# Performance work log

Hardware: AMD Instinct MI355X
Metric: run time of the kernel (lower is better)

Reference implementation:

```python
import jax, jax.numpy as jnp
from jax import lax
import numpy as np

B, T, F, H = 4096, 512, 8, 16  # batch, seq, n_features, hidden_dim


def _lstm(x, Wih, Whh, bih, bhh):
    """PyTorch-convention LSTM over batch-first x [B,T,in].
    Returns (h_T [B,H], outputs [B,T,H]). Gate order: i, f, g, o."""
    Bn = x.shape[0]
    Hn = Whh.shape[1]
    xs = jnp.swapaxes(x, 0, 1)                       # [T,B,in]
    x_proj = xs @ Wih.T + (bih + bhh)                # precompute input GEMM: [T,B,4H]

    def step(carry, xp):
        h, c = carry
        gates = xp + h @ Whh.T                       # [B,4H]
        i, f, g, o = jnp.split(gates, 4, axis=-1)
        i = jax.nn.sigmoid(i)
        f = jax.nn.sigmoid(f)
        g = jnp.tanh(g)
        o = jax.nn.sigmoid(o)
        c = f * c + i * g
        h = o * jnp.tanh(c)
        return (h, c), h

    h0 = jnp.zeros((Bn, Hn), x.dtype)
    (hT, _), hs = lax.scan(step, (h0, h0), x_proj)
    return hT, jnp.swapaxes(hs, 0, 1)                # [B,H], [B,T,H]


def setup_inputs() -> dict:
    key = jax.random.key(0)
    ks = jax.random.split(key, 11)
    s_e = 1.0 / np.sqrt(H)
    u = lambda k, shp: jax.random.uniform(k, shp, jnp.float32, -s_e, s_e)
    return {
        "x": jax.random.normal(ks[0], (B, T, F), jnp.float32),
        "enc_Wih": u(ks[1], (4 * H, F)),
        "enc_Whh": u(ks[2], (4 * H, H)),
        "enc_bih": u(ks[3], (4 * H,)),
        "enc_bhh": u(ks[4], (4 * H,)),
        "dec_Wih": u(ks[5], (4 * H, H)),
        "dec_Whh": u(ks[6], (4 * H, H)),
        "dec_bih": u(ks[7], (4 * H,)),
        "dec_bhh": u(ks[8], (4 * H,)),
        "out_W": u(ks[9], (F, H)),
        "out_b": u(ks[10], (F,)),
    }


def reference(x, enc_Wih, enc_Whh, enc_bih, enc_bhh,
              dec_Wih, dec_Whh, dec_bih, dec_bhh, out_W, out_b):
    # encoder: keep only final hidden state h_T
    hT, _ = _lstm(x, enc_Wih, enc_Whh, enc_bih, enc_bhh)   # [B,H]
    # repeat over time: h.squeeze(0).unsqueeze(1).repeat(1,T,1)
    repeated = jnp.broadcast_to(hT[:, None, :], (x.shape[0], x.shape[1], hT.shape[1]))
    _, decoded = _lstm(repeated, dec_Wih, dec_Whh, dec_bih, dec_bhh)  # [B,T,H]
    return decoded @ out_W.T + out_b                       # [B,T,F]
```

## Files before the change

### kernel.cpp

```cpp
#include <hip/hip_runtime.h>

#define B_ 4096
#define T_ 512
#define F_ 8
#define H_ 16

typedef float f32x2 __attribute__((ext_vector_type(2)));

__device__ __forceinline__ f32x2 pkfma(f32x2 a, f32x2 b, f32x2 c) {
    return __builtin_elementwise_fma(a, b, c);
}

__device__ __forceinline__ float sigf(float v) {
    return __builtin_amdgcn_rcpf(1.0f + __expf(-v));
}
__device__ __forceinline__ float tanh_f(float v) {
    return 2.0f * __builtin_amdgcn_rcpf(1.0f + __expf(-2.0f * v)) - 1.0f;
}

__global__ __launch_bounds__(256, 2) void lstm_ae_kernel(
    const float* __restrict__ x,
    const float* __restrict__ eWih, const float* __restrict__ eWhh,
    const float* __restrict__ ebih, const float* __restrict__ ebhh,
    const float* __restrict__ dWih, const float* __restrict__ dWhh,
    const float* __restrict__ dbih, const float* __restrict__ dbhh,
    const float* __restrict__ oW,   const float* __restrict__ ob,
    float* __restrict__ out)
{
    const int tid = threadIdx.x;
    const int ch  = tid >> 5;
    const int l   = tid & 31;
    const int j   = l & 15;
    const bool lo = (l < 16);
    const int b   = blockIdx.x * 8 + ch;

    __shared__ __align__(16) float hbuf[8][16];
    __shared__ __align__(16) float xsh[8][256];

    const int r0 = l;
    const int r1 = l + 32;
    const float s1 = lo ? 2.0f : 1.0f;
    const float m1 = lo ? 2.0f : 1.0f;
    const float c1 = lo ? -1.0f : 0.0f;

    f32x2 wh0[8], wh1[8], wi0[4], wi1[4];
#pragma unroll
    for (int k = 0; k < 16; k += 4) {
        float4 v0 = *(const float4*)(eWhh + r0 * 16 + k);
        float4 v1 = *(const float4*)(eWhh + r1 * 16 + k);
        wh0[k/2]   = f32x2{v0.x, v0.y}; wh0[k/2+1] = f32x2{v0.z, v0.w};
        wh1[k/2]   = f32x2{v1.x, v1.y}; wh1[k/2+1] = f32x2{v1.z, v1.w};
    }
#pragma unroll
    for (int k = 0; k < 8; k += 4) {
        float4 v0 = *(const float4*)(eWih + r0 * 8 + k);
        float4 v1 = *(const float4*)(eWih + r1 * 8 + k);
        wi0[k/2]   = f32x2{v0.x, v0.y}; wi0[k/2+1] = f32x2{v0.z, v0.w};
        wi1[k/2]   = f32x2{v1.x, v1.y}; wi1[k/2+1] = f32x2{v1.z, v1.w};
    }
    const float bias0 = ebih[r0] + ebhh[r0];
    const float bias1 = ebih[r1] + ebhh[r1];

    float h = 0.0f, c = 0.0f;
    if (lo) hbuf[ch][j] = 0.0f;
    __builtin_amdgcn_wave_barrier();
    f32x2 hb[8];
#pragma unroll
    for (int p = 0; p < 8; ++p) hb[p] = f32x2{0.0f, 0.0f};

    const float* xb = x + (size_t)b * (T_ * F_);

    for (int c0 = 0; c0 < T_; c0 += 32) {
        {
            float4 v0 = *(const float4*)(xb + c0 * F_ + l * 4);
            float4 v1 = *(const float4*)(xb + c0 * F_ + 128 + l * 4);
            *(float4*)&xsh[ch][l * 4]       = v0;
            *(float4*)&xsh[ch][128 + l * 4] = v1;
        }
        __builtin_amdgcn_wave_barrier();
        for (int s = 0; s < 32; ++s) {
            float4 u0 = *(const float4*)&xsh[ch][s * F_];
            float4 u1 = *(const float4*)&xsh[ch][s * F_ + 4];
            f32x2 xv0 = f32x2{u0.x, u0.y}, xv1 = f32x2{u0.z, u0.w};
            f32x2 xv2 = f32x2{u1.x, u1.y}, xv3 = f32x2{u1.z, u1.w};

            f32x2 a0a = f32x2{bias0, 0.0f}, a0b = f32x2{0.0f, 0.0f};
            f32x2 a1a = f32x2{bias1, 0.0f}, a1b = f32x2{0.0f, 0.0f};
            a0a = pkfma(wi0[0], xv0, a0a); a0b = pkfma(wi0[1], xv1, a0b);
            a0a = pkfma(wi0[2], xv2, a0a); a0b = pkfma(wi0[3], xv3, a0b);
            a1a = pkfma(wi1[0], xv0, a1a); a1b = pkfma(wi1[1], xv1, a1b);
            a1a = pkfma(wi1[2], xv2, a1a); a1b = pkfma(wi1[3], xv3, a1b);
#pragma unroll
            for (int p = 0; p < 8; p += 2) {
                a0a = pkfma(wh0[p],   hb[p],   a0a);
                a0b = pkfma(wh0[p+1], hb[p+1], a0b);
                a1a = pkfma(wh1[p],   hb[p],   a1a);
                a1b = pkfma(wh1[p+1], hb[p+1], a1b);
            }
            f32x2 t0 = a0a + a0b; const float acc0 = t0.x + t0.y;
            f32x2 t1 = a1a + a1b; const float acc1 = t1.x + t1.y;

            const float a0 = sigf(acc0);
            const float a1 = m1 * __builtin_amdgcn_rcpf(1.0f + __expf(-s1 * acc1)) + c1;
            const float e0 = __shfl_xor(a0, 16, 64);
            const float e1 = __shfl_xor(a1, 16, 64);
            const float gi = lo ? a0 : e0;
            const float gf = lo ? e0 : a0;
            const float gg = lo ? a1 : e1;
            const float go = lo ? e1 : a1;
            c = gf * c + gi * gg;
            h = go * tanh_f(c);
            __builtin_amdgcn_wave_barrier();
            if (lo) hbuf[ch][j] = h;
            __builtin_amdgcn_wave_barrier();
            float4 q0 = *(const float4*)&hbuf[ch][0];
            float4 q1 = *(const float4*)&hbuf[ch][4];
            float4 q2 = *(const float4*)&hbuf[ch][8];
            float4 q3 = *(const float4*)&hbuf[ch][12];
            hb[0] = f32x2{q0.x, q0.y}; hb[1] = f32x2{q0.z, q0.w};
            hb[2] = f32x2{q1.x, q1.y}; hb[3] = f32x2{q1.z, q1.w};
            hb[4] = f32x2{q2.x, q2.y}; hb[5] = f32x2{q2.z, q2.w};
            hb[6] = f32x2{q3.x, q3.y}; hb[7] = f32x2{q3.z, q3.w};
        }
    }

    f32x2 wd0[8], wd1[8], wo2[8];
    float xp0, xp1;
    {
        f32x2 p0a = f32x2{dbih[r0] + dbhh[r0], 0.0f}, p0b = f32x2{0.0f, 0.0f};
        f32x2 p1a = f32x2{dbih[r1] + dbhh[r1], 0.0f}, p1b = f32x2{0.0f, 0.0f};
#pragma unroll
        for (int k = 0; k < 16; k += 4) {
            float4 v0 = *(const float4*)(dWih + r0 * 16 + k);
            float4 v1 = *(const float4*)(dWih + r1 * 16 + k);
            p0a = pkfma(f32x2{v0.x, v0.y}, hb[k/2],   p0a);
            p0b = pkfma(f32x2{v0.z, v0.w}, hb[k/2+1], p0b);
            p1a = pkfma(f32x2{v1.x, v1.y}, hb[k/2],   p1a);
            p1b = pkfma(f32x2{v1.z, v1.w}, hb[k/2+1], p1b);
        }
        f32x2 t0 = p0a + p0b; xp0 = t0.x + t0.y;
        f32x2 t1 = p1a + p1b; xp1 = t1.x + t1.y;
#pragma unroll
        for (int k = 0; k < 16; k += 4) {
            float4 v0 = *(const float4*)(dWhh + r0 * 16 + k);
            float4 v1 = *(const float4*)(dWhh + r1 * 16 + k);
            wd0[k/2]   = f32x2{v0.x, v0.y}; wd0[k/2+1] = f32x2{v0.z, v0.w};
            wd1[k/2]   = f32x2{v1.x, v1.y}; wd1[k/2+1] = f32x2{v1.z, v1.w};
        }
        const int r = l & 7;
#pragma unroll
        for (int k = 0; k < 16; k += 4) {
            float4 v = *(const float4*)(oW + r * 16 + k);
            wo2[k/2]   = f32x2{v.x, v.y}; wo2[k/2+1] = f32x2{v.z, v.w};
        }
    }
    const float obv = ob[l & 7];

    h = 0.0f; c = 0.0f;
    __builtin_amdgcn_wave_barrier();
    if (lo) hbuf[ch][j] = 0.0f;
    __builtin_amdgcn_wave_barrier();
#pragma unroll
    for (int p = 0; p < 8; ++p) hb[p] = f32x2{0.0f, 0.0f};

    float* outp = out + (size_t)b * (T_ * F_);

    for (int t = 0; t < T_; ++t) {
        f32x2 a0a = f32x2{xp0, 0.0f}, a0b = f32x2{0.0f, 0.0f};
        f32x2 a1a = f32x2{xp1, 0.0f}, a1b = f32x2{0.0f, 0.0f};
#pragma unroll
        for (int p = 0; p < 8; p += 2) {
            a0a = pkfma(wd0[p],   hb[p],   a0a);
            a0b = pkfma(wd0[p+1], hb[p+1], a0b);
            a1a = pkfma(wd1[p],   hb[p],   a1a);
            a1b = pkfma(wd1[p+1], hb[p+1], a1b);
        }
        f32x2 t0 = a0a + a0b; const float acc0 = t0.x + t0.y;
        f32x2 t1 = a1a + a1b; const float acc1 = t1.x + t1.y;

        const float a0 = sigf(acc0);
        const float a1 = m1 * __builtin_amdgcn_rcpf(1.0f + __expf(-s1 * acc1)) + c1;
        const float e0 = __shfl_xor(a0, 16, 64);
        const float e1 = __shfl_xor(a1, 16, 64);
        const float gi = lo ? a0 : e0;
        const float gf = lo ? e0 : a0;
        const float gg = lo ? a1 : e1;
        const float go = lo ? e1 : a1;
        c = gf * c + gi * gg;
        h = go * tanh_f(c);
        __builtin_amdgcn_wave_barrier();
        if (lo) hbuf[ch][j] = h;
        __builtin_amdgcn_wave_barrier();
        float4 q0 = *(const float4*)&hbuf[ch][0];
        float4 q1 = *(const float4*)&hbuf[ch][4];
        float4 q2 = *(const float4*)&hbuf[ch][8];
        float4 q3 = *(const float4*)&hbuf[ch][12];
        hb[0] = f32x2{q0.x, q0.y}; hb[1] = f32x2{q0.z, q0.w};
        hb[2] = f32x2{q1.x, q1.y}; hb[3] = f32x2{q1.z, q1.w};
        hb[4] = f32x2{q2.x, q2.y}; hb[5] = f32x2{q2.z, q2.w};
        hb[6] = f32x2{q3.x, q3.y}; hb[7] = f32x2{q3.z, q3.w};

        f32x2 oaa = f32x2{obv, 0.0f}, oab = f32x2{0.0f, 0.0f};
#pragma unroll
        for (int p = 0; p < 8; p += 2) {
            oaa = pkfma(wo2[p],   hb[p],   oaa);
            oab = pkfma(wo2[p+1], hb[p+1], oab);
        }
        f32x2 to = oaa + oab; const float oa = to.x + to.y;
        if (l < 8) outp[t * F_ + l] = oa;
    }
}

extern "C" void kernel_launch(void* const* d_in, const int* in_sizes, int n_in,
                              void* d_out, int out_size, void* d_ws, size_t ws_size,
                              hipStream_t stream) {
    (void)in_sizes; (void)n_in; (void)d_ws; (void)ws_size; (void)out_size;
    lstm_ae_kernel<<<dim3(B_ / 8), dim3(256), 0, stream>>>(
        (const float*)d_in[0],
        (const float*)d_in[1], (const float*)d_in[2],
        (const float*)d_in[3], (const float*)d_in[4],
        (const float*)d_in[5], (const float*)d_in[6],
        (const float*)d_in[7], (const float*)d_in[8],
        (const float*)d_in[9], (const float*)d_in[10],
        (float*)d_out);
}
```

Measured before the change: 406.3 us.

## Map one gate row per lane with full-wave chains and DPP quad exchange

Each batch chain now uses a full 64-lane wave, one gate row per lane, laid out so the four gates of a hidden unit sit in one quad. Gate values are exchanged with DPP quad permutes instead of cross-half shuffles, which halves the per-lane FMA and exp work on the serial recurrence path. The x chunk for the next step is prefetched into registers, and launch bounds are raised to 4 blocks per CU. The cost is twice as many waves in total for the same batch, so throughput depends on occupancy hiding the latency of the sequential steps.

```diff
diff --git a/kernel.cpp b/kernel.cpp
--- a/kernel.cpp
+++ b/kernel.cpp
@@ -11,14 +11,18 @@
     return __builtin_elementwise_fma(a, b, c);
 }
 
-__device__ __forceinline__ float sigf(float v) {
-    return __builtin_amdgcn_rcpf(1.0f + __expf(-v));
-}
 __device__ __forceinline__ float tanh_f(float v) {
     return 2.0f * __builtin_amdgcn_rcpf(1.0f + __expf(-2.0f * v)) - 1.0f;
 }
 
-__global__ __launch_bounds__(256, 2) void lstm_ae_kernel(
+template <int CTRL>
+__device__ __forceinline__ float qperm(float v) {
+    int i = __builtin_bit_cast(int, v);
+    int rr = __builtin_amdgcn_update_dpp(i, i, CTRL, 0xF, 0xF, false);
+    return __builtin_bit_cast(float, rr);
+}
+
+__global__ __launch_bounds__(256, 4) void lstm_ae_kernel(
     const float* __restrict__ x,
     const float* __restrict__ eWih, const float* __restrict__ eWhh,
     const float* __restrict__ ebih, const float* __restrict__ ebhh,
@@ -28,90 +32,76 @@
     float* __restrict__ out)
 {
     const int tid = threadIdx.x;
-    const int ch  = tid >> 5;
-    const int l   = tid & 31;
-    const int j   = l & 15;
-    const bool lo = (l < 16);
-    const int b   = blockIdx.x * 8 + ch;
-
-    __shared__ __align__(16) float hbuf[8][16];
-    __shared__ __align__(16) float xsh[8][256];
-
-    const int r0 = l;
-    const int r1 = l + 32;
-    const float s1 = lo ? 2.0f : 1.0f;
-    const float m1 = lo ? 2.0f : 1.0f;
-    const float c1 = lo ? -1.0f : 0.0f;
-
-    f32x2 wh0[8], wh1[8], wi0[4], wi1[4];
+    const int ch  = tid >> 6;
+    const int l   = tid & 63;
+    const int g   = l & 3;
+    const int j   = l >> 2;
+    const int r   = g * 16 + j;
+    const int b   = blockIdx.x * 4 + ch;
+
+    __shared__ __align__(16) float hbuf[4][16];
+    __shared__ __align__(16) float xsh[4][256];
+
+    const bool g0 = (g == 0);
+    const float s1 = (g == 2) ? 2.0f : 1.0f;
+    const float m1 = (g == 2) ? 2.0f : 1.0f;
+    const float c1 = (g == 2) ? -1.0f : 0.0f;
+
+    f32x2 wh[8], wi[4];
 #pragma unroll
     for (int k = 0; k < 16; k += 4) {
-        float4 v0 = *(const float4*)(eWhh + r0 * 16 + k);
-        float4 v1 = *(const float4*)(eWhh + r1 * 16 + k);
-        wh0[k/2]   = f32x2{v0.x, v0.y}; wh0[k/2+1] = f32x2{v0.z, v0.w};
-        wh1[k/2]   = f32x2{v1.x, v1.y}; wh1[k/2+1] = f32x2{v1.z, v1.w};
+        float4 v = *(const float4*)(eWhh + r * 16 + k);
+        wh[k/2]   = f32x2{v.x, v.y}; wh[k/2+1] = f32x2{v.z, v.w};
     }
 #pragma unroll
     for (int k = 0; k < 8; k += 4) {
-        float4 v0 = *(const float4*)(eWih + r0 * 8 + k);
-        float4 v1 = *(const float4*)(eWih + r1 * 8 + k);
-        wi0[k/2]   = f32x2{v0.x, v0.y}; wi0[k/2+1] = f32x2{v0.z, v0.w};
-        wi1[k/2]   = f32x2{v1.x, v1.y}; wi1[k/2+1] = f32x2{v1.z, v1.w};
-    }
-    const float bias0 = ebih[r0] + ebhh[r0];
-    const float bias1 = ebih[r1] + ebhh[r1];
-
-    float h = 0.0f, c = 0.0f;
-    if (lo) hbuf[ch][j] = 0.0f;
+        float4 v = *(const float4*)(eWih + r * 8 + k);
+        wi[k/2]   = f32x2{v.x, v.y}; wi[k/2+1] = f32x2{v.z, v.w};
+    }
+    const float bias = ebih[r] + ebhh[r];
+
+    float c = 0.0f;
+    f32x2 hb[8];
+#pragma unroll
+    for (int p = 0; p < 8; ++p) hb[p] = f32x2{0.0f, 0.0f};
+    if (l < 16) hbuf[ch][l] = 0.0f;
     __builtin_amdgcn_wave_barrier();
-    f32x2 hb[8];
-#pragma unroll
-    for (int p = 0; p < 8; ++p) hb[p] = f32x2{0.0f, 0.0f};
 
     const float* xb = x + (size_t)b * (T_ * F_);
+    float4 nx = *(const float4*)(xb + l * 4);
 
     for (int c0 = 0; c0 < T_; c0 += 32) {
-        {
-            float4 v0 = *(const float4*)(xb + c0 * F_ + l * 4);
-            float4 v1 = *(const float4*)(xb + c0 * F_ + 128 + l * 4);
-            *(float4*)&xsh[ch][l * 4]       = v0;
-            *(float4*)&xsh[ch][128 + l * 4] = v1;
-        }
-        __builtin_amdgcn_wave_barrier();
+        __builtin_amdgcn_wave_barrier();
+        *(float4*)&xsh[ch][l * 4] = nx;
+        __builtin_amdgcn_wave_barrier();
+        if (c0 + 32 < T_)
+            nx = *(const float4*)(xb + (c0 + 32) * F_ + l * 4);
         for (int s = 0; s < 32; ++s) {
             float4 u0 = *(const float4*)&xsh[ch][s * F_];
             float4 u1 = *(const float4*)&xsh[ch][s * F_ + 4];
-            f32x2 xv0 = f32x2{u0.x, u0.y}, xv1 = f32x2{u0.z, u0.w};
-            f32x2 xv2 = f32x2{u1.x, u1.y}, xv3 = f32x2{u1.z, u1.w};
-
-            f32x2 a0a = f32x2{bias0, 0.0f}, a0b = f32x2{0.0f, 0.0f};
-            f32x2 a1a = f32x2{bias1, 0.0f}, a1b = f32x2{0.0f, 0.0f};
-            a0a = pkfma(wi0[0], xv0, a0a); a0b = pkfma(wi0[1], xv1, a0b);
-            a0a = pkfma(wi0[2], xv2, a0a); a0b = pkfma(wi0[3], xv3, a0b);
-            a1a = pkfma(wi1[0], xv0, a1a); a1b = pkfma(wi1[1], xv1, a1b);
-            a1a = pkfma(wi1[2], xv2, a1a); a1b = pkfma(wi1[3], xv3, a1b);
+
+            f32x2 aa = f32x2{bias, 0.0f}, ab = f32x2{0.0f, 0.0f};
+            aa = pkfma(wi[0], f32x2{u0.x, u0.y}, aa);
+            ab = pkfma(wi[1], f32x2{u0.z, u0.w}, ab);
+            aa = pkfma(wi[2], f32x2{u1.x, u1.y}, aa);
+            ab = pkfma(wi[3], f32x2{u1.z, u1.w}, ab);
 #pragma unroll
             for (int p = 0; p < 8; p += 2) {
-                a0a = pkfma(wh0[p],   hb[p],   a0a);
-                a0b = pkfma(wh0[p+1], hb[p+1], a0b);
-                a1a = pkfma(wh1[p],   hb[p],   a1a);
-                a1b = pkfma(wh1[p+1], hb[p+1], a1b);
+                aa = pkfma(wh[p],   hb[p],   aa);
+                ab = pkfma(wh[p+1], hb[p+1], ab);
             }
-            f32x2 t0 = a0a + a0b; const float acc0 = t0.x + t0.y;
-            f32x2 t1 = a1a + a1b; const float acc1 = t1.x + t1.y;
-
-            const float a0 = sigf(acc0);
-            const float a1 = m1 * __builtin_amdgcn_rcpf(1.0f + __expf(-s1 * acc1)) + c1;
-            const float e0 = __shfl_xor(a0, 16, 64);
-            const float e1 = __shfl_xor(a1, 16, 64);
-            const float gi = lo ? a0 : e0;
-            const float gf = lo ? e0 : a0;
-            const float gg = lo ? a1 : e1;
-            const float go = lo ? e1 : a1;
-            c = gf * c + gi * gg;
-            h = go * tanh_f(c);
+            f32x2 t = aa + ab;
+            const float acc = t.x + t.y;
+
+            const float a  = m1 * __builtin_amdgcn_rcpf(1.0f + __expf(-s1 * acc)) + c1;
+            const float e1 = qperm<0xB1>(a);
+            const float e2 = qperm<0x4E>(a);
+            const float e3 = qperm<0xB1>(e2);
+            c = e1 * c + a * e2;
+            const float h = e3 * tanh_f(c);
+
             __builtin_amdgcn_wave_barrier();
-            if (lo) hbuf[ch][j] = h;
+            if (g0) hbuf[ch][j] = h;
             __builtin_amdgcn_wave_barrier();
             float4 q0 = *(const float4*)&hbuf[ch][0];
             float4 q1 = *(const float4*)&hbuf[ch][4];
@@ -124,72 +114,57 @@
         }
     }
 
-    f32x2 wd0[8], wd1[8], wo2[8];
-    float xp0, xp1;
+    f32x2 wd[8], wo2[8];
+    float xp;
     {
-        f32x2 p0a = f32x2{dbih[r0] + dbhh[r0], 0.0f}, p0b = f32x2{0.0f, 0.0f};
-        f32x2 p1a = f32x2{dbih[r1] + dbhh[r1], 0.0f}, p1b = f32x2{0.0f, 0.0f};
+        f32x2 pa = f32x2{dbih[r] + dbhh[r], 0.0f}, pb = f32x2{0.0f, 0.0f};
 #pragma unroll
         for (int k = 0; k < 16; k += 4) {
-            float4 v0 = *(const float4*)(dWih + r0 * 16 + k);
-            float4 v1 = *(const float4*)(dWih + r1 * 16 + k);
-            p0a = pkfma(f32x2{v0.x, v0.y}, hb[k/2],   p0a);
-            p0b = pkfma(f32x2{v0.z, v0.w}, hb[k/2+1], p0b);
-            p1a = pkfma(f32x2{v1.x, v1.y}, hb[k/2],   p1a);
-            p1b = pkfma(f32x2{v1.z, v1.w}, hb[k/2+1], p1b);
-        }
-        f32x2 t0 = p0a + p0b; xp0 = t0.x + t0.y;
-        f32x2 t1 = p1a + p1b; xp1 = t1.x + t1.y;
+            float4 v = *(const float4*)(dWih + r * 16 + k);
+            pa = pkfma(f32x2{v.x, v.y}, hb[k/2],   pa);
+            pb = pkfma(f32x2{v.z, v.w}, hb[k/2+1], pb);
+        }
+        f32x2 t = pa + pb; xp = t.x + t.y;
 #pragma unroll
         for (int k = 0; k < 16; k += 4) {
-            float4 v0 = *(const float4*)(dWhh + r0 * 16 + k);
-            float4 v1 = *(const float4*)(dWhh + r1 * 16 + k);
-            wd0[k/2]   = f32x2{v0.x, v0.y}; wd0[k/2+1] = f32x2{v0.z, v0.w};
-            wd1[k/2]   = f32x2{v1.x, v1.y}; wd1[k/2+1] = f32x2{v1.z, v1.w};
-        }
-        const int r = l & 7;
+            float4 v = *(const float4*)(dWhh + r * 16 + k);
+            wd[k/2]   = f32x2{v.x, v.y}; wd[k/2+1] = f32x2{v.z, v.w};
+        }
+        const int fo = l & 7;
 #pragma unroll
         for (int k = 0; k < 16; k += 4) {
-            float4 v = *(const float4*)(oW + r * 16 + k);
+            float4 v = *(const float4*)(oW + fo * 16 + k);
             wo2[k/2]   = f32x2{v.x, v.y}; wo2[k/2+1] = f32x2{v.z, v.w};
         }
     }
     const float obv = ob[l & 7];
 
-    h = 0.0f; c = 0.0f;
+    c = 0.0f;
+#pragma unroll
+    for (int p = 0; p < 8; ++p) hb[p] = f32x2{0.0f, 0.0f};
     __builtin_amdgcn_wave_barrier();
-    if (lo) hbuf[ch][j] = 0.0f;
-    __builtin_amdgcn_wave_barrier();
-#pragma unroll
-    for (int p = 0; p < 8; ++p) hb[p] = f32x2{0.0f, 0.0f};
 
     float* outp = out + (size_t)b * (T_ * F_);
 
     for (int t = 0; t < T_; ++t) {
-        f32x2 a0a = f32x2{xp0, 0.0f}, a0b = f32x2{0.0f, 0.0f};
-        f32x2 a1a = f32x2{xp1, 0.0f}, a1b = f32x2{0.0f, 0.0f};
+        f32x2 aa = f32x2{xp, 0.0f}, ab = f32x2{0.0f, 0.0f};
 #pragma unroll
         for (int p = 0; p < 8; p += 2) {
-            a0a = pkfma(wd0[p],   hb[p],   a0a);
-            a0b = pkfma(wd0[p+1], hb[p+1], a0b);
-            a1a = pkfma(wd1[p],   hb[p],   a1a);
-            a1b = pkfma(wd1[p+1], hb[p+1], a1b);
-        }
-        f32x2 t0 = a0a + a0b; const float acc0 = t0.x + t0.y;
-        f32x2 t1 = a1a + a1b; const float acc1 = t1.x + t1.y;
-
-        const float a0 = sigf(acc0);
-        const float a1 = m1 * __builtin_amdgcn_rcpf(1.0f + __expf(-s1 * acc1)) + c1;
-        const float e0 = __shfl_xor(a0, 16, 64);
-        const float e1 = __shfl_xor(a1, 16, 64);
-        const float gi = lo ? a0 : e0;
-        const float gf = lo ? e0 : a0;
-        const float gg = lo ? a1 : e1;
-        const float go = lo ? e1 : a1;
-        c = gf * c + gi * gg;
-        h = go * tanh_f(c);
-        __builtin_amdgcn_wave_barrier();
-        if (lo) hbuf[ch][j] = h;
+            aa = pkfma(wd[p],   hb[p],   aa);
+            ab = pkfma(wd[p+1], hb[p+1], ab);
+        }
+        f32x2 tt = aa + ab;
+        const float acc = tt.x + tt.y;
+
+        const float a  = m1 * __builtin_amdgcn_rcpf(1.0f + __expf(-s1 * acc)) + c1;
+        const float e1 = qperm<0xB1>(a);
+        const float e2 = qperm<0x4E>(a);
+        const float e3 = qperm<0xB1>(e2);
+        c = e1 * c + a * e2;
+        const float h = e3 * tanh_f(c);
+
+        __builtin_amdgcn_wave_barrier();
+        if (g0) hbuf[ch][j] = h;
         __builtin_amdgcn_wave_barrier();
         float4 q0 = *(const float4*)&hbuf[ch][0];
         float4 q1 = *(const float4*)&hbuf[ch][4];
@@ -206,8 +181,8 @@
             oaa = pkfma(wo2[p],   hb[p],   oaa);
             oab = pkfma(wo2[p+1], hb[p+1], oab);
         }
-        f32x2 to = oaa + oab; const float oa = to.x + to.y;
-        if (l < 8) outp[t * F_ + l] = oa;
+        f32x2 to = oaa + oab;
+        if (l < 8) outp[t * F_ + l] = to.x + to.y;
     }
 }
 
@@ -215,7 +190,7 @@
                               void* d_out, int out_size, void* d_ws, size_t ws_size,
                               hipStream_t stream) {
     (void)in_sizes; (void)n_in; (void)d_ws; (void)ws_size; (void)out_size;
-    lstm_ae_kernel<<<dim3(B_ / 8), dim3(256), 0, stream>>>(
+    lstm_ae_kernel<<<dim3(B_ / 4), dim3(256), 0, stream>>>(
         (const float*)d_in[0],
         (const float*)d_in[1], (const float*)d_in[2],
         (const float*)d_in[3], (const float*)d_in[4],
```

Result: slower. 440.5 us (+8.4%).
